# Performance work log

Hardware: AMD Instinct MI355X
Metric: run time of the kernel (lower is better)

Reference implementation:

```python
import jax, jax.numpy as jnp
import numpy as np

# Per-feature MLP topology from NAM._get_topology: 1->32->64->128->64->32->16->1
DIMS = [1, 32, 64, 128, 64, 32, 16, 1]
N_LAYERS = len(DIMS) - 1  # 7 linear layers
BATCH, DIM = 2048, 256


def setup_inputs() -> dict:
    key = jax.random.key(0)
    inp = {"x": jax.random.normal(jax.random.fold_in(key, 0), (BATCH, DIM), dtype=jnp.float32)}
    # Batched parameters: stack the `dim` independent tiny MLPs along a leading axis.
    # torch.nn.Linear default init: U(-1/sqrt(fan_in), 1/sqrt(fan_in)) for W and b.
    for l in range(N_LAYERS):
        fi, fo = DIMS[l], DIMS[l + 1]
        kw, kb = jax.random.split(jax.random.fold_in(key, l + 1))
        bound = 1.0 / np.sqrt(fi)
        inp[f"W{l}"] = jax.random.uniform(kw, (DIM, fi, fo), jnp.float32, -bound, bound)
        inp[f"b{l}"] = jax.random.uniform(kb, (DIM, fo), jnp.float32, -bound, bound)
    return inp


def reference(x, W0, b0, W1, b1, W2, b2, W3, b3, W4, b4, W5, b5, W6, b6):
    Ws = [W0, W1, W2, W3, W4, W5, W6]
    bs = [b0, b1, b2, b3, b4, b5, b6]
    # h: [batch, dim, feat] — all `dim` tiny MLPs run as one batched GEMM per layer
    h = x[:, :, None]
    for l in range(N_LAYERS):
        h = jnp.einsum('bdi,dio->bdo', h, Ws[l]) + bs[l][None, :, :]
        if l < N_LAYERS - 1:
            h = jax.nn.relu(h)
    # funcs_sum = sum over features of each per-feature scalar output -> [batch, 1]
    return jnp.sum(h, axis=1)
```

## Files before the change

kernel.cpp:

```cpp
#include <hip/hip_runtime.h>

#define BATCH 2048
#define DIM   256

typedef _Float16 half8 __attribute__((ext_vector_type(8)));
typedef __attribute__((ext_vector_type(4))) float f32x4;

#define NTILES 41
#define TILE_HALVES 512

#define P_W0 0
#define P_B0 32
#define P_W6 64
#define P_B1 80
#define P_B2 144
#define P_B3 272
#define P_B4 336
#define P_B5 368
#define P_B6 384
#define P_TOT 385

struct Frag { half8 k0, k1, k2, k3; };

__device__ __forceinline__ half8 relu_pack(f32x4 e, f32x4 o) {
  half8 r;
#pragma unroll
  for (int j = 0; j < 4; ++j) {
    r[j]     = (_Float16)fmaxf(e[j], 0.0f);
    r[4 + j] = (_Float16)fmaxf(o[j], 0.0f);
  }
  return r;
}

template <int KT>
__device__ __forceinline__ f32x4 chain(const _Float16* __restrict__ tb,
                                       const Frag& a, f32x4 c) {
  c = __builtin_amdgcn_mfma_f32_16x16x32_f16(*(const half8*)tb, a.k0, c, 0, 0, 0);
  if constexpr (KT > 1)
    c = __builtin_amdgcn_mfma_f32_16x16x32_f16(*(const half8*)(tb + TILE_HALVES),
                                               a.k1, c, 0, 0, 0);
  if constexpr (KT > 2) {
    c = __builtin_amdgcn_mfma_f32_16x16x32_f16(
        *(const half8*)(tb + 2 * TILE_HALVES), a.k2, c, 0, 0, 0);
    c = __builtin_amdgcn_mfma_f32_16x16x32_f16(
        *(const half8*)(tb + 3 * TILE_HALVES), a.k3, c, 0, 0, 0);
  }
  return c;
}

template <int KT, int TBASE, int PB>
__device__ __forceinline__ void ntp_pair(
    const _Float16* __restrict__ packs, const float* __restrict__ pl, int lane,
    int q, const Frag& a0, const Frag& a1, const Frag& a2, const Frag& a3,
    half8& r0, half8& r1, half8& r2, half8& r3) {
  const f32x4 bias0 = *(const f32x4*)(pl + PB + (q << 2));
  const f32x4 bias1 = *(const f32x4*)(pl + PB + 16 + (q << 2));
  const _Float16* tb0 = packs + (size_t)TBASE * TILE_HALVES + lane * 8;
  const _Float16* tb1 = tb0 + (size_t)KT * TILE_HALVES;
  const f32x4 c00 = chain<KT>(tb0, a0, bias0);
  const f32x4 c01 = chain<KT>(tb0, a1, bias0);
  const f32x4 c02 = chain<KT>(tb0, a2, bias0);
  const f32x4 c03 = chain<KT>(tb0, a3, bias0);
  const f32x4 c10 = chain<KT>(tb1, a0, bias1);
  const f32x4 c11 = chain<KT>(tb1, a1, bias1);
  const f32x4 c12 = chain<KT>(tb1, a2, bias1);
  const f32x4 c13 = chain<KT>(tb1, a3, bias1);
  r0 = relu_pack(c00, c10);
  r1 = relu_pack(c01, c11);
  r2 = relu_pack(c02, c12);
  r3 = relu_pack(c03, c13);
}

template <int FI, int FO, int LBASE, int PBIAS>
__device__ __forceinline__ void layerX(
    const _Float16* __restrict__ packs, const float* __restrict__ pl, int lane,
    int q, const Frag& a0, const Frag& a1, const Frag& a2, const Frag& a3,
    Frag& o0, Frag& o1, Frag& o2, Frag& o3) {
  constexpr int KT = FI / 32, NTP = FO / 32;
  ntp_pair<KT, LBASE + 0 * 2 * KT, PBIAS + 0 * 32>(
      packs, pl, lane, q, a0, a1, a2, a3, o0.k0, o1.k0, o2.k0, o3.k0);
  if constexpr (NTP > 1)
    ntp_pair<KT, LBASE + 1 * 2 * KT, PBIAS + 1 * 32>(
        packs, pl, lane, q, a0, a1, a2, a3, o0.k1, o1.k1, o2.k1, o3.k1);
  if constexpr (NTP > 2) {
    ntp_pair<KT, LBASE + 2 * 2 * KT, PBIAS + 2 * 32>(
        packs, pl, lane, q, a0, a1, a2, a3, o0.k2, o1.k2, o2.k2, o3.k2);
    ntp_pair<KT, LBASE + 3 * 2 * KT, PBIAS + 3 * 32>(
        packs, pl, lane, q, a0, a1, a2, a3, o0.k3, o1.k3, o2.k3, o3.k3);
  }
}

__global__ __launch_bounds__(1024) void mlp_fused(
    const float* __restrict__ x,
    const float* __restrict__ W0, const float* __restrict__ b0,
    const float* __restrict__ W1, const float* __restrict__ b1,
    const float* __restrict__ W2, const float* __restrict__ b2,
    const float* __restrict__ W3, const float* __restrict__ b3,
    const float* __restrict__ W4, const float* __restrict__ b4,
    const float* __restrict__ W5, const float* __restrict__ b5,
    const float* __restrict__ W6, const float* __restrict__ b6,
    float* __restrict__ partial) {
  const int t = threadIdx.x;
  const int lane = t & 63;
  const int wave = t >> 6;
  const int m = lane & 15, q = lane >> 4;
  const int d = blockIdx.x;

  __shared__ __align__(16) _Float16 packs[NTILES * TILE_HALVES];
  __shared__ __align__(16) float xs[2048];
  __shared__ __align__(16) float pl[P_TOT];

  for (int i = t; i < 2048; i += 1024)
    xs[i] = x[(size_t)i * DIM + d];

  for (int job = t; job < NTILES * 16; job += 1024) {
    const int tile = job >> 4, sub = job & 15;
    const int jq = sub >> 2, jm4 = sub & 3;
    const float* W; int FI, FO, lt;
    if (tile < 4)       { W = W1; FI = 32;  FO = 64;  lt = tile; }
    else if (tile < 20) { W = W2; FI = 64;  FO = 128; lt = tile - 4; }
    else if (tile < 36) { W = W3; FI = 128; FO = 64;  lt = tile - 20; }
    else if (tile < 40) { W = W4; FI = 64;  FO = 32;  lt = tile - 36; }
    else                { W = W5; FI = 32;  FO = 16;  lt = 0; }
    const int KT = FI >> 5;
    const int mt = lt / KT, kt = lt - mt * KT;
    const float* Wp = W + (size_t)d * FI * FO +
                      (size_t)(kt * 32 + 4 * jq) * FO + mt * 16 + jm4 * 4;
    const f32x4 v0 = *(const f32x4*)(Wp + (size_t)0 * FO);
    const f32x4 v1 = *(const f32x4*)(Wp + (size_t)1 * FO);
    const f32x4 v2 = *(const f32x4*)(Wp + (size_t)2 * FO);
    const f32x4 v3 = *(const f32x4*)(Wp + (size_t)3 * FO);
    const f32x4 v4 = *(const f32x4*)(Wp + (size_t)16 * FO);
    const f32x4 v5 = *(const f32x4*)(Wp + (size_t)17 * FO);
    const f32x4 v6 = *(const f32x4*)(Wp + (size_t)18 * FO);
    const f32x4 v7 = *(const f32x4*)(Wp + (size_t)19 * FO);
    _Float16* pb =
        packs + (size_t)tile * TILE_HALVES + (size_t)(jq * 16 + jm4 * 4) * 8;
#pragma unroll
    for (int c = 0; c < 4; ++c) {
      half8 h;
      h[0] = (_Float16)v0[c];
      h[1] = (_Float16)v1[c];
      h[2] = (_Float16)v2[c];
      h[3] = (_Float16)v3[c];
      h[4] = (_Float16)v4[c];
      h[5] = (_Float16)v5[c];
      h[6] = (_Float16)v6[c];
      h[7] = (_Float16)v7[c];
      *(half8*)(pb + c * 8) = h;
    }
  }
  for (int i = t; i < P_TOT; i += 1024) {
    float v;
    if (i < 32)       v = W0[d * 32 + i];
    else if (i < 64)  v = b0[d * 32 + i - 32];
    else if (i < 80)  v = W6[d * 16 + i - 64];
    else if (i < 144) v = b1[d * 64 + i - 80];
    else if (i < 272) v = b2[d * 128 + i - 144];
    else if (i < 336) v = b3[d * 64 + i - 272];
    else if (i < 368) v = b4[d * 32 + i - 336];
    else if (i < 384) v = b5[d * 16 + i - 368];
    else              v = b6[d];
    pl[i] = v;
  }

  __syncthreads();

  Frag pA0, pA1, pA2, pA3, pB0, pB1, pB2, pB3;

  for (int it = 0; it < 2; ++it) {
    asm volatile("" ::: "memory");

    const int row0 = it * 1024 + wave * 64;

    const f32x4 w0a = *(const f32x4*)(pl + P_W0 + 4 * q);
    const f32x4 w0b = *(const f32x4*)(pl + P_W0 + 16 + 4 * q);
    const f32x4 b0a = *(const f32x4*)(pl + P_B0 + 4 * q);
    const f32x4 b0b = *(const f32x4*)(pl + P_B0 + 16 + 4 * q);

    {
      const int xb = row0 + m;
      const float xv0 = xs[xb];
      const float xv1 = xs[xb + 16];
      const float xv2 = xs[xb + 32];
      const float xv3 = xs[xb + 48];
      half8 h0, h1, h2, h3;
#pragma unroll
      for (int j = 0; j < 4; ++j) {
        h0[j]     = (_Float16)fmaxf(fmaf(xv0, w0a[j], b0a[j]), 0.0f);
        h0[4 + j] = (_Float16)fmaxf(fmaf(xv0, w0b[j], b0b[j]), 0.0f);
        h1[j]     = (_Float16)fmaxf(fmaf(xv1, w0a[j], b0a[j]), 0.0f);
        h1[4 + j] = (_Float16)fmaxf(fmaf(xv1, w0b[j], b0b[j]), 0.0f);
        h2[j]     = (_Float16)fmaxf(fmaf(xv2, w0a[j], b0a[j]), 0.0f);
        h2[4 + j] = (_Float16)fmaxf(fmaf(xv2, w0b[j], b0b[j]), 0.0f);
        h3[j]     = (_Float16)fmaxf(fmaf(xv3, w0a[j], b0a[j]), 0.0f);
        h3[4 + j] = (_Float16)fmaxf(fmaf(xv3, w0b[j], b0b[j]), 0.0f);
      }
      pA0.k0 = h0;
      pA1.k0 = h1;
      pA2.k0 = h2;
      pA3.k0 = h3;
    }

    layerX<32, 64, 0, P_B1>(packs, pl, lane, q,
                            pA0, pA1, pA2, pA3, pB0, pB1, pB2, pB3);
    layerX<64, 128, 4, P_B2>(packs, pl, lane, q,
                             pB0, pB1, pB2, pB3, pA0, pA1, pA2, pA3);
    layerX<128, 64, 20, P_B3>(packs, pl, lane, q,
                              pA0, pA1, pA2, pA3, pB0, pB1, pB2, pB3);
    layerX<64, 32, 36, P_B4>(packs, pl, lane, q,
                             pB0, pB1, pB2, pB3, pA0, pA1, pA2, pA3);

    const f32x4 bias5 = *(const f32x4*)(pl + P_B5 + 4 * q);
    const f32x4 w6v = *(const f32x4*)(pl + P_W6 + 4 * q);
    const float bias6 = pl[P_B6];
    const half8 wf5 =
        *(const half8*)(packs + (size_t)40 * TILE_HALVES + lane * 8);

    const f32x4 a50 = __builtin_amdgcn_mfma_f32_16x16x32_f16(
        wf5, pA0.k0, bias5, 0, 0, 0);
    const f32x4 a51 = __builtin_amdgcn_mfma_f32_16x16x32_f16(
        wf5, pA1.k0, bias5, 0, 0, 0);
    const f32x4 a52 = __builtin_amdgcn_mfma_f32_16x16x32_f16(
        wf5, pA2.k0, bias5, 0, 0, 0);
    const f32x4 a53 = __builtin_amdgcn_mfma_f32_16x16x32_f16(
        wf5, pA3.k0, bias5, 0, 0, 0);
    float v0 = 0.0f, v1 = 0.0f, v2 = 0.0f, v3 = 0.0f;
#pragma unroll
    for (int r = 0; r < 4; ++r) {
      v0 += fmaxf(a50[r], 0.0f) * w6v[r];
      v1 += fmaxf(a51[r], 0.0f) * w6v[r];
      v2 += fmaxf(a52[r], 0.0f) * w6v[r];
      v3 += fmaxf(a53[r], 0.0f) * w6v[r];
    }
    v0 += __shfl_xor(v0, 16);
    v0 += __shfl_xor(v0, 32);
    v1 += __shfl_xor(v1, 16);
    v1 += __shfl_xor(v1, 32);
    v2 += __shfl_xor(v2, 16);
    v2 += __shfl_xor(v2, 32);
    v3 += __shfl_xor(v3, 16);
    v3 += __shfl_xor(v3, 32);
    if (q == 0) {
      partial[(size_t)d * BATCH + row0 + m]      = v0 + bias6;
      partial[(size_t)d * BATCH + row0 + 16 + m] = v1 + bias6;
      partial[(size_t)d * BATCH + row0 + 32 + m] = v2 + bias6;
      partial[(size_t)d * BATCH + row0 + 48 + m] = v3 + bias6;
    }
  }
}

__global__ __launch_bounds__(256) void reduce_kernel(
    const float* __restrict__ partial, float* __restrict__ out) {
  const int b = blockIdx.x * blockDim.x + threadIdx.x;
  float s = 0.0f;
#pragma unroll 8
  for (int d = 0; d < DIM; ++d) s += partial[(size_t)d * BATCH + b];
  out[b] = s;
}

extern "C" void kernel_launch(void* const* d_in, const int* in_sizes, int n_in,
                              void* d_out, int out_size, void* d_ws, size_t ws_size,
                              hipStream_t stream) {
  const float* x = (const float*)d_in[0];
  const float* W[7];
  const float* B[7];
  for (int l = 0; l < 7; ++l) {
    W[l] = (const float*)d_in[1 + 2 * l];
    B[l] = (const float*)d_in[2 + 2 * l];
  }
  float* partial = (float*)d_ws;

  mlp_fused<<<dim3(DIM), dim3(1024), 0, stream>>>(
      x, W[0], B[0], W[1], B[1], W[2], B[2], W[3], B[3], W[4], B[4], W[5], B[5],
      W[6], B[6], partial);

  reduce_kernel<<<dim3(BATCH / 256), dim3(256), 0, stream>>>(partial,
                                                             (float*)d_out);
}
```

Measured before the change: 132.4 us.

## Fuse final feature reduction into MLP kernel via global atomic grid barrier

Drops the separate reduce kernel. Each block signals completion on a global atomic counter and spins until all 256 blocks are done, then reduces 8 batch outputs across the 256 features using shared memory. This removes one kernel launch and its gap but adds a memset and a grid-wide spin barrier. The barrier depends on all 256 blocks being co-resident, which should hold on 256 CUs but is not guaranteed.

```diff
diff --git a/kernel.cpp b/kernel.cpp
--- a/kernel.cpp
+++ b/kernel.cpp
@@ -99,7 +99,8 @@
     const float* __restrict__ W4, const float* __restrict__ b4,
     const float* __restrict__ W5, const float* __restrict__ b5,
     const float* __restrict__ W6, const float* __restrict__ b6,
-    float* __restrict__ partial) {
+    float* __restrict__ partial, int* __restrict__ counter,
+    float* __restrict__ out) {
   const int t = threadIdx.x;
   const int lane = t & 63;
   const int wave = t >> 6;
@@ -109,6 +110,7 @@
   __shared__ __align__(16) _Float16 packs[NTILES * TILE_HALVES];
   __shared__ __align__(16) float xs[2048];
   __shared__ __align__(16) float pl[P_TOT];
+  __shared__ __align__(16) float red[128][8];
 
   for (int i = t; i < 2048; i += 1024)
     xs[i] = x[(size_t)i * DIM + d];
@@ -248,15 +250,28 @@
       partial[(size_t)d * BATCH + row0 + 48 + m] = v3 + bias6;
     }
   }
-}
-
-__global__ __launch_bounds__(256) void reduce_kernel(
-    const float* __restrict__ partial, float* __restrict__ out) {
-  const int b = blockIdx.x * blockDim.x + threadIdx.x;
-  float s = 0.0f;
-#pragma unroll 8
-  for (int d = 0; d < DIM; ++d) s += partial[(size_t)d * BATCH + b];
-  out[b] = s;
+
+  __threadfence();
+  if (t == 0) {
+    __hip_atomic_fetch_add(counter, 1, __ATOMIC_ACQ_REL,
+                           __HIP_MEMORY_SCOPE_AGENT);
+    while (__hip_atomic_load(counter, __ATOMIC_ACQUIRE,
+                             __HIP_MEMORY_SCOPE_AGENT) < DIM)
+      __builtin_amdgcn_s_sleep(2);
+  }
+  __syncthreads();
+  __threadfence();
+
+  const int dg = t >> 3, bl = t & 7;
+  const int bout = d * 8 + bl;
+  red[dg][bl] = partial[(size_t)(dg * 2) * BATCH + bout] +
+                partial[(size_t)(dg * 2 + 1) * BATCH + bout];
+  __syncthreads();
+  if (t < 8) {
+    float acc = 0.0f;
+    for (int j = 0; j < 128; ++j) acc += red[j][t];
+    out[d * 8 + t] = acc;
+  }
 }
 
 extern "C" void kernel_launch(void* const* d_in, const int* in_sizes, int n_in,
@@ -269,12 +284,13 @@
     W[l] = (const float*)d_in[1 + 2 * l];
     B[l] = (const float*)d_in[2 + 2 * l];
   }
-  float* partial = (float*)d_ws;
+  char* ws = (char*)d_ws;
+  float* partial = (float*)ws;
+  int* counter = (int*)(ws + (4 << 20));
+
+  hipMemsetAsync(counter, 0, sizeof(int), stream);
 
   mlp_fused<<<dim3(DIM), dim3(1024), 0, stream>>>(
       x, W[0], B[0], W[1], B[1], W[2], B[2], W[3], B[3], W[4], B[4], W[5], B[5],
-      W[6], B[6], partial);
-
-  reduce_kernel<<<dim3(BATCH / 256), dim3(256), 0, stream>>>(partial,
-                                                             (float*)d_out);
-}
+      W[6], B[6], partial, counter, (float*)d_out);
+}
```

After: 259.2 us. 95.8% more time.
